# Optimization experiments

Hardware: AMD Instinct MI355X
Metric: run time of the kernel (lower is better)

Reference implementation:

```python
import jax, jax.numpy as jnp
import numpy as np

B, TIN, IN, TRI, D, FFN, L, OUT = 8, 1040, 80, 128, 512, 2048, 8, 1024
H, DH, STRIDE, SEG, RC, LC, MAXMEM = 8, 64, 4, 16, 4, 32, 4
NEG = -1e8
SCALE = DH ** -0.5


def _layer_norm(x, g, b, eps=1e-5):
    m = jnp.mean(x, -1, keepdims=True)
    v = jnp.var(x, -1, keepdims=True)
    return (x - m) * jax.lax.rsqrt(v + eps) * g + b


def _build_attention_mask(U, nseg):
    # Faithful port of Emformer._gen_attention_mask; True = masked out.
    rct = RC * nseg
    mlen = nseg - 1
    rc_rows, q_rows, s_rows = [], [], []
    for i in range(nseg):
        rs, re = i * RC, i * RC + RC
        ss, se = max(i * SEG - LC, 0), min((i + 1) * SEG, U)
        ms = max(i - MAXMEM, 0)
        widths = [ms, i - ms, mlen - i, rs, RC, rct - re, ss, se - ss, U - se]

        def row(allowed):
            return np.concatenate([np.full(max(w, 0), j in allowed, dtype=bool)
                                   for j, w in enumerate(widths)])

        r = row({1, 4, 7})  # memory, own rc block, own (left-extended) segment
        rc_rows.append(np.tile(r, (RC, 1)))
        q_rows.append(np.tile(r, (min(SEG, U - i * SEG), 1)))
        s_rows.append(row({4, 7})[None])  # summary: rc block + segment only
    allow = np.concatenate([np.concatenate(rc_rows), np.concatenate(q_rows), np.concatenate(s_rows)])
    return jnp.asarray(~allow)


def _forward(input, lengths, w_in, ln_in_g, ln_in_b, wq, bq, wk, bk, wv, bv, wo, bo,
             ff_ln_g, ff_ln_b, w1, b1, w2, b2, ln_out_g, ln_out_b, w_out, b_out, lng, lnb):
    x = input @ w_in                                    # (B, TIN, TRI) input_linear (no bias)
    nb, t, _ = x.shape
    nf = t - t % STRIDE
    x = x[:, :nf].reshape(nb, nf // STRIDE, TRI * STRIDE)  # time reduction -> (B, Tr, D)
    lr = lengths // STRIDE
    x = jnp.transpose(x, (1, 0, 2))                     # (Tr, B, D) time-major like torch Emformer
    Tr = x.shape[0]
    U = Tr - RC                                         # utterance length (256)
    nseg = -(-U // SEG)
    utt = x[:U]
    # right-context blocks: hard-copied per segment (last block = trailing rc)
    starts = np.concatenate([np.arange(1, nseg) * SEG, [Tr - RC]])
    idx = (starts[:, None] + np.arange(RC)[None, :]).reshape(-1)
    rc = x[idx]                                         # (nseg*RC, B, D)
    Rt = rc.shape[0]
    Q = Rt + U + nseg                                   # rc + utterance + summary queries
    K = (nseg - 1) + Rt + U                             # mems + rc + utterance keys
    attn_mask = _build_attention_mask(U, nseg)          # (Q, K)
    mems0 = utt.reshape(nseg, SEG, nb, D).mean(1)[:-1]  # AvgPool1d(seg) on raw utterance, drop last
    # padding mask over keys (faithful to _gen_padding_mask)
    rcbl = Q - jnp.max(lr) - nseg
    klen = lr + (nseg - 1) + rcbl
    pad = jnp.arange(K)[None, :] >= klen[:, None]       # (B, K), True = masked

    def step(carry, p):
        utt, rc, mems = carry
        g1, be1, Wq, Bq, Wk, Bk, Wv, Bv, Wo, Bo, g2, be2, Wf1, Bf1, Wf2, Bf2, g3, be3 = p
        ln = _layer_norm(jnp.concatenate([rc, utt]), g1, be1)
        ln_rc, ln_utt = ln[:Rt], ln[Rt:]
        summary = ln_utt.reshape(nseg, SEG, nb, D).mean(1)       # (nseg, B, D)
        qin = jnp.concatenate([ln_rc, ln_utt, summary])          # (Q, B, D)
        kin = jnp.concatenate([mems, ln_rc, ln_utt])             # (K, B, D)
        q = (qin @ Wq + Bq).reshape(Q, nb, H, DH)
        k = (kin @ Wk + Bk).reshape(K, nb, H, DH)
        v = (kin @ Wv + Bv).reshape(K, nb, H, DH)
        w = jnp.einsum('qbhd,kbhd->bhqk', q * SCALE, k)
        w = jnp.where(attn_mask[None, None], NEG, w)
        w = jnp.where(pad[:, None, None, :], NEG, w)
        probs = jax.nn.softmax(w, axis=-1)
        att = jnp.einsum('bhqk,kbhd->qbhd', probs, v).reshape(Q, nb, D)
        out = att @ Wo + Bo
        rcu = out[:Rt + U]
        new_mems = jnp.tanh(out[Rt + U:])[:-1]                   # tanh_on_mem=True, drop last summary
        res = rcu + jnp.concatenate([rc, utt])                   # residual w/ pre-LN input
        h = _layer_norm(res, g2, be2)
        h = jax.nn.relu(h @ Wf1 + Bf1) @ Wf2 + Bf2               # pos_ff (pre-LN inside)
        res = res + h
        res = _layer_norm(res, g3, be3)
        return (res[Rt:], res[:Rt], new_mems), None

    xs = (ln_in_g, ln_in_b, wq, bq, wk, bk, wv, bv, wo, bo,
          ff_ln_g, ff_ln_b, w1, b1, w2, b2, ln_out_g, ln_out_b)
    (utt, rc, mems), _ = jax.lax.scan(step, (utt, rc, mems0), xs)
    y = jnp.transpose(utt, (1, 0, 2))                   # (B, U, D)
    y = _layer_norm(y @ w_out + b_out, lng, lnb)        # output_linear + LayerNorm
    return y, lr


def setup_inputs() -> dict:
    key = jax.random.key(0)
    ks = jax.random.split(key, 12)

    def w(k, shape, fan):
        return jax.random.normal(k, shape, jnp.float32) / np.sqrt(fan)

    return {
        "input": jax.random.normal(ks[0], (B, TIN, IN), jnp.float32),
        "lengths": jax.random.randint(ks[1], (B,), 256, 1025, jnp.int32),
        "w_in": w(ks[2], (IN, TRI), IN),
        "ln_in_g": jnp.ones((L, D), jnp.float32), "ln_in_b": jnp.zeros((L, D), jnp.float32),
        "wq": w(ks[3], (L, D, D), D), "bq": jnp.zeros((L, D), jnp.float32),
        "wk": w(ks[4], (L, D, D), D), "bk": jnp.zeros((L, D), jnp.float32),
        "wv": w(ks[5], (L, D, D), D), "bv": jnp.zeros((L, D), jnp.float32),
        "wo": w(ks[6], (L, D, D), D), "bo": jnp.zeros((L, D), jnp.float32),
        "ff_ln_g": jnp.ones((L, D), jnp.float32), "ff_ln_b": jnp.zeros((L, D), jnp.float32),
        "w1": w(ks[7], (L, D, FFN), D), "b1": jnp.zeros((L, FFN), jnp.float32),
        "w2": w(ks[8], (L, FFN, D), FFN), "b2": jnp.zeros((L, D), jnp.float32),
        "ln_out_g": jnp.ones((L, D), jnp.float32), "ln_out_b": jnp.zeros((L, D), jnp.float32),
        "w_out": w(ks[9], (D, OUT), D), "b_out": jnp.zeros((OUT,), jnp.float32),
        "lng": jnp.ones((OUT,), jnp.float32), "lnb": jnp.zeros((OUT,), jnp.float32),
    }


def reference(input, lengths, w_in, ln_in_g, ln_in_b, wq, bq, wk, bk, wv, bv, wo, bo,
              ff_ln_g, ff_ln_b, w1, b1, w2, b2, ln_out_g, ln_out_b, w_out, b_out, lng, lnb):
    return _forward(input, lengths, w_in, ln_in_g, ln_in_b, wq, bq, wk, bk, wv, bv, wo, bo,
                    ff_ln_g, ff_ln_b, w1, b1, w2, b2, ln_out_g, ln_out_b, w_out, b_out, lng, lnb)
```

## Files before the change

### kernel.cpp

```cpp
#include <hip/hip_runtime.h>
#include <math.h>

#define NB 8
#define D 512
#define H 8
#define DH 64
#define NSEG 16
#define RT 64
#define UU 256
#define QN 336
#define KN 335
#define SROWS 320
#define FFN_D 2048
#define LAYERS 8
#define OUTD 1024
#define TR 260
#define NEGV (-100000000.0f)
#define QSCALE 0.125f

typedef __attribute__((ext_vector_type(8))) short bf16x8;
typedef __attribute__((ext_vector_type(4))) float f32x4;

__device__ inline unsigned short f2bf(float f) {
    union { float f; unsigned int u; } v; v.f = f;
    unsigned int u = v.u;
    unsigned int r = (u + 0x7FFFu + ((u >> 16) & 1u)) >> 16;
    return (unsigned short)r;
}
__device__ inline float bf2f(unsigned short h) {
    union { unsigned int u; float f; } v; v.u = ((unsigned int)h) << 16;
    return v.f;
}

__global__ void lr_k(const int* __restrict__ lengths, int* __restrict__ lrw,
                     float* __restrict__ out_lr) {
    if (threadIdx.x == 0) {
        int mx = 0;
        for (int b = 0; b < NB; ++b) {
            int v = lengths[b] >> 2;
            lrw[b] = v;
            out_lr[b] = (float)v;
            if (v > mx) mx = v;
        }
        lrw[NB] = mx;
    }
}

__global__ __launch_bounds__(128) void inproj_k(const float* __restrict__ input,
                                                const float* __restrict__ w_in,
                                                float* __restrict__ XB) {
    __shared__ float wl[80 * 128];
    __shared__ float il[4 * 80];
    int tid = threadIdx.x;
    int t = blockIdx.x >> 3;
    int b = blockIdx.x & 7;
    for (int i = tid; i < 80 * 128; i += 128) wl[i] = w_in[i];
    const float* inp = input + ((size_t)b * 1040 + (size_t)t * 4) * 80;
    for (int i = tid; i < 320; i += 128) il[i] = inp[i];
    __syncthreads();
    float* xrow = XB + ((size_t)(t * NB + b)) * D;
#pragma unroll
    for (int c = 0; c < 4; ++c) {
        float acc = 0.f;
        for (int i = 0; i < 80; ++i) acc = fmaf(il[c * 80 + i], wl[i * 128 + tid], acc);
        xrow[c * 128 + tid] = acc;
    }
}

__global__ __launch_bounds__(256) void initstate_k(const float* __restrict__ XB,
                                                   float* __restrict__ S) {
    int r = blockIdx.x;
    int srow = r >> 3, b = r & 7;
    int src;
    if (srow < RT) {
        int i = srow >> 2, jj = srow & 3;
        src = (i < 15 ? (i + 1) * 16 : 256) + jj;
    } else {
        src = srow - RT;
    }
    const float* xr = XB + ((size_t)(src * NB + b)) * D;
    float* sr = S + (size_t)r * D;
    sr[threadIdx.x] = xr[threadIdx.x];
    sr[threadIdx.x + 256] = xr[threadIdx.x + 256];
}

__global__ __launch_bounds__(256) void mems0_k(const float* __restrict__ XB,
                                               unsigned short* __restrict__ MEMS) {
    int ib = blockIdx.x;
    int i = ib >> 3, b = ib & 7;
    for (int c = 0; c < 2; ++c) {
        int col = threadIdx.x + c * 256;
        float s = 0.f;
#pragma unroll
        for (int t = 0; t < 16; ++t) s += XB[((size_t)((i * 16 + t) * NB + b)) * D + col];
        MEMS[(size_t)ib * D + col] = f2bf(s * (1.f / 16.f));
    }
}

__global__ __launch_bounds__(256) void ln_k(const float* __restrict__ X,
                                            unsigned short* __restrict__ Y16,
                                            float* __restrict__ Yf,
                                            const float* __restrict__ g,
                                            const float* __restrict__ be, int dual) {
    int row = blockIdx.x;
    const float* x = X + (size_t)row * D;
    float v[2];
    float s = 0.f, ss = 0.f;
#pragma unroll
    for (int j = 0; j < 2; ++j) {
        v[j] = x[threadIdx.x + j * 256];
        s += v[j];
        ss = fmaf(v[j], v[j], ss);
    }
#pragma unroll
    for (int off = 32; off; off >>= 1) {
        s += __shfl_xor(s, off);
        ss += __shfl_xor(ss, off);
    }
    __shared__ float rs_[4], rss_[4];
    int w = threadIdx.x >> 6;
    if ((threadIdx.x & 63) == 0) {
        rs_[w] = s;
        rss_[w] = ss;
    }
    __syncthreads();
    s = rs_[0] + rs_[1] + rs_[2] + rs_[3];
    ss = rss_[0] + rss_[1] + rss_[2] + rss_[3];
    float mean = s * (1.f / D);
    float var = ss * (1.f / D) - mean * mean;
    float rstd = rsqrtf(var + 1e-5f);
#pragma unroll
    for (int j = 0; j < 2; ++j) {
        int col = threadIdx.x + j * 256;
        float y = (v[j] - mean) * rstd * g[col] + be[col];
        Y16[(size_t)row * D + col] = f2bf(y);
        if (dual) Yf[(size_t)row * D + col] = y;
    }
}

__global__ __launch_bounds__(256) void ln_res_k(const float* __restrict__ OUTB,
                                                float* __restrict__ SB,
                                                unsigned short* __restrict__ MEMS,
                                                unsigned short* __restrict__ Y16,
                                                const float* __restrict__ g,
                                                const float* __restrict__ be) {
    int row = blockIdx.x;
    if (row >= SROWS * NB) {
        int j = row - SROWS * NB;
#pragma unroll
        for (int c = 0; c < 2; ++c) {
            int col = threadIdx.x + c * 256;
            MEMS[(size_t)j * D + col] = f2bf(tanhf(OUTB[(size_t)row * D + col]));
        }
        return;
    }
    float v[2];
    float s = 0.f, ss = 0.f;
#pragma unroll
    for (int j = 0; j < 2; ++j) {
        int col = threadIdx.x + j * 256;
        float r = SB[(size_t)row * D + col] + OUTB[(size_t)row * D + col];
        SB[(size_t)row * D + col] = r;
        v[j] = r;
        s += r;
        ss = fmaf(r, r, ss);
    }
#pragma unroll
    for (int off = 32; off; off >>= 1) {
        s += __shfl_xor(s, off);
        ss += __shfl_xor(ss, off);
    }
    __shared__ float rs_[4], rss_[4];
    int w = threadIdx.x >> 6;
    if ((threadIdx.x & 63) == 0) {
        rs_[w] = s;
        rss_[w] = ss;
    }
    __syncthreads();
    s = rs_[0] + rs_[1] + rs_[2] + rs_[3];
    ss = rss_[0] + rss_[1] + rss_[2] + rss_[3];
    float mean = s * (1.f / D);
    float var = ss * (1.f / D) - mean * mean;
    float rstd = rsqrtf(var + 1e-5f);
#pragma unroll
    for (int j = 0; j < 2; ++j) {
        int col = threadIdx.x + j * 256;
        Y16[(size_t)row * D + col] = f2bf((v[j] - mean) * rstd * g[col] + be[col]);
    }
}

__global__ __launch_bounds__(256) void summary_k(const unsigned short* __restrict__ LN16,
                                                 unsigned short* __restrict__ SUM16) {
    int ib = blockIdx.x;
    int i = ib >> 3, b = ib & 7;
    for (int c = 0; c < 2; ++c) {
        int col = threadIdx.x + c * 256;
        float s = 0.f;
#pragma unroll
        for (int t = 0; t < 16; ++t)
            s += bf2f(LN16[((size_t)((RT + i * 16 + t) * NB + b)) * D + col]);
        SUM16[(size_t)ib * D + col] = f2bf(s * (1.f / 16.f));
    }
}

__device__ inline void conv_tile(float (*tile)[33], const float* __restrict__ src, int srcN,
                                 int k0, int sn0, unsigned short* __restrict__ dst, int dstK,
                                 int dn0) {
    int t = threadIdx.x;
    int r = t >> 3, c4 = (t & 7) * 4;
    float4 v = *(const float4*)&src[(size_t)(k0 + r) * srcN + sn0 + c4];
    tile[r][c4 + 0] = v.x;
    tile[r][c4 + 1] = v.y;
    tile[r][c4 + 2] = v.z;
    tile[r][c4 + 3] = v.w;
    __syncthreads();
    ushort4 o;
    o.x = f2bf(tile[c4 + 0][r]);
    o.y = f2bf(tile[c4 + 1][r]);
    o.z = f2bf(tile[c4 + 2][r]);
    o.w = f2bf(tile[c4 + 3][r]);
    *(ushort4*)&dst[(size_t)(dn0 + r) * dstK + k0 + c4] = o;
}

__global__ __launch_bounds__(256) void convw_k(const float* __restrict__ wq,
                                               const float* __restrict__ wk,
                                               const float* __restrict__ wv,
                                               const float* __restrict__ wo,
                                               const float* __restrict__ w1,
                                               const float* __restrict__ w2,
                                               const float* __restrict__ bq,
                                               const float* __restrict__ bk,
                                               const float* __restrict__ bv,
                                               unsigned short* __restrict__ WQKV,
                                               unsigned short* __restrict__ WO16,
                                               unsigned short* __restrict__ W1T,
                                               unsigned short* __restrict__ W2T,
                                               float* __restrict__ BQKV, int l) {
    __shared__ float tile[32][33];
    int t = blockIdx.x;
    if (t == 0) {
        for (int i = threadIdx.x; i < 1536; i += 256)
            BQKV[i] = i < 512 ? bq[l * 512 + i]
                              : (i < 1024 ? bk[l * 512 + i - 512] : bv[l * 512 + i - 1024]);
    }
    if (t < 768) {
        int tn = t % 48, tk = t / 48;
        int n0 = tn * 32, k0 = tk * 32;
        const float* src;
        int sn0;
        if (n0 < 512) { src = wq + (size_t)l * 262144; sn0 = n0; }
        else if (n0 < 1024) { src = wk + (size_t)l * 262144; sn0 = n0 - 512; }
        else { src = wv + (size_t)l * 262144; sn0 = n0 - 1024; }
        conv_tile(tile, src, 512, k0, sn0, WQKV, 512, n0);
    } else if (t < 1024) {
        int tt = t - 768;
        int n0 = (tt % 16) * 32, k0 = (tt / 16) * 32;
        conv_tile(tile, wo + (size_t)l * 262144, 512, k0, n0, WO16, 512, n0);
    } else if (t < 2048) {
        int tt = t - 1024;
        int n0 = (tt % 64) * 32, k0 = (tt / 64) * 32;
        conv_tile(tile, w1 + (size_t)l * 1048576, 2048, k0, n0, W1T, 512, n0);
    } else {
        int tt = t - 2048;
        int n0 = (tt % 16) * 32, k0 = (tt / 16) * 32;
        conv_tile(tile, w2 + (size_t)l * 1048576, 512, k0, n0, W2T, 2048, n0);
    }
}

__global__ __launch_bounds__(256) void convout_k(const float* __restrict__ w_out,
                                                 unsigned short* __restrict__ WOUT16) {
    __shared__ float tile[32][33];
    int t = blockIdx.x;
    int n0 = (t % 32) * 32, k0 = (t / 32) * 32;
    conv_tile(tile, w_out, 1024, k0, n0, WOUT16, 512, n0);
}

__global__ __launch_bounds__(256) void gemm16_k(const unsigned short* __restrict__ A,
                                                const unsigned short* __restrict__ BT,
                                                const float* __restrict__ bias,
                                                void* __restrict__ Cp, int M, int N, int K,
                                                int Kchunk, int flags) {
    __shared__ unsigned short As[2][64][40];
    __shared__ unsigned short Bs[2][64][40];
    int tid = threadIdx.x;
    int wave = tid >> 6, lane = tid & 63;
    int wm = wave >> 1, wn = wave & 1;
    int quad = lane >> 4, sub = lane & 15;
    int m0 = blockIdx.y * 64, n0 = blockIdx.x * 64;
    int kb = blockIdx.z * Kchunk, ke = kb + Kchunk;

    int lrow = tid >> 3, lkc = tid & 7;
    int lrow2 = lrow + 32;
    int lkh = lkc >> 2, lkl = lkc & 3;

    f32x4 acc[2][2] = {};
    int4 ar0, ar1, br0, br1;

    auto loadT = [&](int k0) {
        int gr0 = m0 + lrow, gr1 = m0 + lrow2;
        ar0 = (gr0 < M) ? *(const int4*)&A[(size_t)gr0 * K + k0 + lkc * 8] : make_int4(0, 0, 0, 0);
        ar1 = (gr1 < M) ? *(const int4*)&A[(size_t)gr1 * K + k0 + lkc * 8] : make_int4(0, 0, 0, 0);
        br0 = *(const int4*)&BT[(size_t)(n0 + lrow) * K + k0 + lkc * 8];
        br1 = *(const int4*)&BT[(size_t)(n0 + lrow2) * K + k0 + lkc * 8];
    };
    auto storeT = [&]() {
        *(int4*)&As[lkh][lrow][lkl * 8] = ar0;
        *(int4*)&As[lkh][lrow2][lkl * 8] = ar1;
        *(int4*)&Bs[lkh][lrow][lkl * 8] = br0;
        *(int4*)&Bs[lkh][lrow2][lkl * 8] = br1;
    };
    auto compute = [&]() {
#pragma unroll
        for (int ks = 0; ks < 2; ++ks) {
            bf16x8 af[2], bf[2];
#pragma unroll
            for (int mi = 0; mi < 2; ++mi)
                af[mi] = *(const bf16x8*)&As[ks][wm * 32 + mi * 16 + sub][quad * 8];
#pragma unroll
            for (int ni = 0; ni < 2; ++ni)
                bf[ni] = *(const bf16x8*)&Bs[ks][wn * 32 + ni * 16 + sub][quad * 8];
#pragma unroll
            for (int mi = 0; mi < 2; ++mi)
#pragma unroll
                for (int ni = 0; ni < 2; ++ni)
                    acc[mi][ni] = __builtin_amdgcn_mfma_f32_16x16x32_bf16(af[mi], bf[ni],
                                                                          acc[mi][ni], 0, 0, 0);
        }
    };

    loadT(kb);
    storeT();
    __syncthreads();
    for (int k0 = kb + 64; k0 < ke; k0 += 64) {
        loadT(k0);
        compute();
        __syncthreads();
        storeT();
        __syncthreads();
    }
    compute();

    bool relu = flags & 1, addc = flags & 2, obf = flags & 4, atom = flags & 8;
    bool addbias = !atom || blockIdx.z == 0;
    float* Cf = (float*)Cp;
    unsigned short* Ch = (unsigned short*)Cp;
#pragma unroll
    for (int mi = 0; mi < 2; ++mi) {
#pragma unroll
        for (int ni = 0; ni < 2; ++ni) {
#pragma unroll
            for (int r = 0; r < 4; ++r) {
                int row = m0 + wm * 32 + mi * 16 + quad * 4 + r;
                int col = n0 + wn * 32 + ni * 16 + sub;
                if (row < M) {
                    float v = acc[mi][ni][r] + (addbias ? bias[col] : 0.f);
                    if (relu) v = fmaxf(v, 0.f);
                    size_t idx = (size_t)row * N + col;
                    if (obf) {
                        Ch[idx] = f2bf(v);
                    } else if (atom) {
                        atomicAdd(&Cf[idx], v);
                    } else {
                        if (addc) v += Cf[idx];
                        Cf[idx] = v;
                    }
                }
            }
        }
    }
}

__global__ __launch_bounds__(64) void attn_k(const unsigned short* __restrict__ QKV,
                                             unsigned short* __restrict__ ATT,
                                             const int* __restrict__ lrw) {
    int lane = threadIdx.x;
    int qrow = blockIdx.x;
    int bh = blockIdx.y;
    int b = bh >> 3, h = bh & 7;

    int i, is_sum;
    if (qrow < RT) {
        i = qrow >> 2;
        is_sum = 0;
    } else if (qrow < RT + UU) {
        i = (qrow - RT) >> 4;
        is_sum = 0;
    } else {
        i = qrow - (RT + UU);
        is_sum = 1;
    }
    int ms = (i > 4) ? (i - 4) : 0;
    int n_mem = is_sum ? 0 : (i - ms);
    int us = (i * 16 - 32 > 0) ? (i * 16 - 32) : 0;
    int ue = (i + 1) * 16;
    int total = n_mem + 4 + (ue - us);
    int klen = KN + lrw[b] - lrw[NB];

    __shared__ float qs[64];
    __shared__ float ps[64];
    __shared__ int kks[64];
    qs[lane] = bf2f(QKV[(size_t)(120 + qrow * NB + b) * 1536 + h * DH + lane]) * QSCALE;
    __syncthreads();

    int kk = -1;
    if (lane < total) {
        if (lane < n_mem)
            kk = ms + lane;
        else if (lane < n_mem + 4)
            kk = 15 + i * 4 + (lane - n_mem);
        else
            kk = 79 + us + (lane - n_mem - 4);
    }
    float s = NEGV;
    if (kk >= 0 && kk < klen) {
        const int4* kr = (const int4*)&QKV[(size_t)(kk * NB + b) * 1536 + 512 + h * DH];
        float accd = 0.f;
#pragma unroll
        for (int c = 0; c < 8; ++c) {
            int4 kv = kr[c];
            const int uu[4] = {kv.x, kv.y, kv.z, kv.w};
#pragma unroll
            for (int j = 0; j < 4; ++j) {
                float lo = __uint_as_float(((unsigned)uu[j]) << 16);
                float hi = __uint_as_float(((unsigned)uu[j]) & 0xFFFF0000u);
                accd = fmaf(lo, qs[c * 8 + j * 2], accd);
                accd = fmaf(hi, qs[c * 8 + j * 2 + 1], accd);
            }
        }
        s = accd;
    }
    float m = s;
#pragma unroll
    for (int off = 32; off; off >>= 1) m = fmaxf(m, __shfl_xor(m, off));
    float p = __expf(s - m);
    float sum = p;
#pragma unroll
    for (int off = 32; off; off >>= 1) sum += __shfl_xor(sum, off);
    float inv = 1.f / sum;
    ps[lane] = p * inv;
    kks[lane] = kk;
    __syncthreads();

    float acc = 0.f;
    for (int j = 0; j < total; ++j) {
        int kkj = kks[j];
        acc = fmaf(ps[j], bf2f(QKV[(size_t)(kkj * NB + b) * 1536 + 1024 + h * DH + lane]), acc);
    }
    ATT[(size_t)(qrow * NB + b) * D + h * DH + lane] = f2bf(acc);
}

__global__ __launch_bounds__(256) void final_ln_k(const float* __restrict__ Yb,
                                                  const float* __restrict__ g,
                                                  const float* __restrict__ be,
                                                  float* __restrict__ out) {
    int row = blockIdx.x;
    int u = row >> 3, b = row & 7;
    const float* x = Yb + (size_t)row * OUTD;
    float v[4];
    float s = 0.f, ss = 0.f;
#pragma unroll
    for (int j = 0; j < 4; ++j) {
        v[j] = x[threadIdx.x + j * 256];
        s += v[j];
        ss = fmaf(v[j], v[j], ss);
    }
#pragma unroll
    for (int off = 32; off; off >>= 1) {
        s += __shfl_xor(s, off);
        ss += __shfl_xor(ss, off);
    }
    __shared__ float rs_[4], rss_[4];
    int w = threadIdx.x >> 6;
    if ((threadIdx.x & 63) == 0) {
        rs_[w] = s;
        rss_[w] = ss;
    }
    __syncthreads();
    s = rs_[0] + rs_[1] + rs_[2] + rs_[3];
    ss = rss_[0] + rss_[1] + rss_[2] + rss_[3];
    float mean = s * (1.f / OUTD);
    float var = ss * (1.f / OUTD) - mean * mean;
    float rstd = rsqrtf(var + 1e-5f);
    float* o = out + ((size_t)(b * 256 + u)) * OUTD;
#pragma unroll
    for (int j = 0; j < 4; ++j) {
        int col = threadIdx.x + j * 256;
        o[col] = (v[j] - mean) * rstd * g[col] + be[col];
    }
}

extern "C" void kernel_launch(void* const* d_in, const int* in_sizes, int n_in, void* d_out,
                              int out_size, void* d_ws, size_t ws_size, hipStream_t stream) {
    (void)in_sizes;
    (void)n_in;
    (void)out_size;
    (void)ws_size;
    const float* input = (const float*)d_in[0];
    const int* lengths = (const int*)d_in[1];
    const float* w_in = (const float*)d_in[2];
    const float* ln_in_g = (const float*)d_in[3];
    const float* ln_in_b = (const float*)d_in[4];
    const float* wq = (const float*)d_in[5];
    const float* bq = (const float*)d_in[6];
    const float* wk = (const float*)d_in[7];
    const float* bk = (const float*)d_in[8];
    const float* wv = (const float*)d_in[9];
    const float* bv = (const float*)d_in[10];
    const float* wo = (const float*)d_in[11];
    const float* bo = (const float*)d_in[12];
    const float* ff_g = (const float*)d_in[13];
    const float* ff_b = (const float*)d_in[14];
    const float* w1 = (const float*)d_in[15];
    const float* b1 = (const float*)d_in[16];
    const float* w2 = (const float*)d_in[17];
    const float* b2 = (const float*)d_in[18];
    const float* lo_g = (const float*)d_in[19];
    const float* lo_b = (const float*)d_in[20];
    const float* w_out = (const float*)d_in[21];
    const float* b_out = (const float*)d_in[22];
    const float* lng = (const float*)d_in[23];
    const float* lnb = (const float*)d_in[24];
    float* out = (float*)d_out;

    char* wsc = (char*)d_ws;
    size_t off = 0;
    auto alloc = [&](size_t bytes) {
        char* p = wsc + off;
        off += (bytes + 255) & ~(size_t)255;
        return p;
    };
    unsigned short* ACT16 = (unsigned short*)alloc(2808ULL * 512 * 2);
    unsigned short* ATT16 = (unsigned short*)alloc(2688ULL * 512 * 2);
    unsigned short* HB16 = (unsigned short*)alloc(2560ULL * 2048 * 2);
    unsigned short* QKVB = (unsigned short*)alloc(2808ULL * 1536 * 2);
    float* SB = (float*)alloc(2560ULL * 512 * 4);
    unsigned short* WQKV16 = (unsigned short*)alloc(1536ULL * 512 * 2);
    unsigned short* WO16 = (unsigned short*)alloc(512ULL * 512 * 2);
    unsigned short* W1T = (unsigned short*)alloc(2048ULL * 512 * 2);
    unsigned short* W2T = (unsigned short*)alloc(512ULL * 2048 * 2);
    unsigned short* WOUT16 = (unsigned short*)alloc(1024ULL * 512 * 2);
    float* BQKV = (float*)alloc(1536 * 4);
    int* LRW = (int*)alloc(64);

    unsigned short* MEMS16 = ACT16;
    unsigned short* LNB16 = ACT16 + 120 * 512;
    unsigned short* SUMB16 = ACT16 + 2680 * 512;
    float* XB = (float*)QKVB;
    float* OUTB = (float*)QKVB;
    float* HBf = (float*)QKVB;

    lr_k<<<1, 64, 0, stream>>>(lengths, LRW, out + (size_t)NB * 256 * 1024);
    convout_k<<<512, 256, 0, stream>>>(w_out, WOUT16);
    inproj_k<<<TR * NB, 128, 0, stream>>>(input, w_in, XB);
    initstate_k<<<SROWS * NB, 256, 0, stream>>>(XB, SB);
    mems0_k<<<15 * NB, 256, 0, stream>>>(XB, MEMS16);

    for (int l = 0; l < LAYERS; ++l) {
        convw_k<<<3072, 256, 0, stream>>>(wq, wk, wv, wo, w1, w2, bq, bk, bv, WQKV16, WO16, W1T,
                                          W2T, BQKV, l);
        ln_k<<<SROWS * NB, 256, 0, stream>>>(SB, LNB16, SB, ln_in_g + l * D, ln_in_b + l * D, 0);
        summary_k<<<NSEG * NB, 256, 0, stream>>>(LNB16, SUMB16);
        gemm16_k<<<dim3(24, 44, 1), 256, 0, stream>>>(ACT16, WQKV16, BQKV, QKVB, 2808, 1536, 512,
                                                      512, 4);
        attn_k<<<dim3(QN, NB * H), 64, 0, stream>>>(QKVB, ATT16, LRW);
        gemm16_k<<<dim3(8, 42, 1), 256, 0, stream>>>(ATT16, WO16, bo + l * D, OUTB, QN * NB, D,
                                                     D, D, 0);
        ln_res_k<<<(SROWS + 15) * NB, 256, 0, stream>>>(OUTB, SB, MEMS16, LNB16, ff_g + l * D,
                                                        ff_b + l * D);
        gemm16_k<<<dim3(32, 40, 1), 256, 0, stream>>>(LNB16, W1T, b1 + l * FFN_D, HB16,
                                                      SROWS * NB, FFN_D, D, D, 1 | 4);
        gemm16_k<<<dim3(8, 40, 4), 256, 0, stream>>>(HB16, W2T, b2 + l * D, SB, SROWS * NB, D,
                                                     FFN_D, 512, 8);
        ln_k<<<SROWS * NB, 256, 0, stream>>>(SB, LNB16, SB, lo_g + l * D, lo_b + l * D, 1);
    }
    gemm16_k<<<dim3(16, 32, 1), 256, 0, stream>>>(LNB16 + (size_t)RT * NB * D, WOUT16, b_out,
                                                  HBf, UU * NB, OUTD, D, D, 0);
    final_ln_k<<<UU * NB, 256, 0, stream>>>(HBf, lng, lnb, out);
}
```

Before: 1.276 ms.

## Merge all heads into one 256-thread attention block per query row and batch

After: 1.196 ms. 6.3% less time.

```diff
diff --git a/kernel.cpp b/kernel.cpp
--- a/kernel.cpp
+++ b/kernel.cpp
@@ -370,13 +370,12 @@
     }
 }
 
-__global__ __launch_bounds__(64) void attn_k(const unsigned short* __restrict__ QKV,
-                                             unsigned short* __restrict__ ATT,
-                                             const int* __restrict__ lrw) {
-    int lane = threadIdx.x;
+__global__ __launch_bounds__(256) void attn_k(const unsigned short* __restrict__ QKV,
+                                              unsigned short* __restrict__ ATT,
+                                              const int* __restrict__ lrw) {
+    int tid = threadIdx.x;
     int qrow = blockIdx.x;
-    int bh = blockIdx.y;
-    int b = bh >> 3, h = bh & 7;
+    int b = blockIdx.y;
 
     int i, is_sum;
     if (qrow < RT) {
@@ -396,57 +395,93 @@
     int total = n_mem + 4 + (ue - us);
     int klen = KN + lrw[b] - lrw[NB];
 
-    __shared__ float qs[64];
-    __shared__ float ps[64];
+    __shared__ float qs[512];
+    __shared__ float sc[H][64];
     __shared__ int kks[64];
-    qs[lane] = bf2f(QKV[(size_t)(120 + qrow * NB + b) * 1536 + h * DH + lane]) * QSCALE;
-    __syncthreads();
-
-    int kk = -1;
-    if (lane < total) {
-        if (lane < n_mem)
-            kk = ms + lane;
-        else if (lane < n_mem + 4)
-            kk = 15 + i * 4 + (lane - n_mem);
-        else
-            kk = 79 + us + (lane - n_mem - 4);
-    }
-    float s = NEGV;
-    if (kk >= 0 && kk < klen) {
-        const int4* kr = (const int4*)&QKV[(size_t)(kk * NB + b) * 1536 + 512 + h * DH];
-        float accd = 0.f;
-#pragma unroll
-        for (int c = 0; c < 8; ++c) {
-            int4 kv = kr[c];
-            const int uu[4] = {kv.x, kv.y, kv.z, kv.w};
-#pragma unroll
-            for (int j = 0; j < 4; ++j) {
-                float lo = __uint_as_float(((unsigned)uu[j]) << 16);
-                float hi = __uint_as_float(((unsigned)uu[j]) & 0xFFFF0000u);
-                accd = fmaf(lo, qs[c * 8 + j * 2], accd);
-                accd = fmaf(hi, qs[c * 8 + j * 2 + 1], accd);
+
+    {
+        const unsigned int* qrp =
+            (const unsigned int*)&QKV[(size_t)(120 + qrow * NB + b) * 1536];
+        unsigned int u = qrp[tid];
+        qs[2 * tid] = __uint_as_float(u << 16) * QSCALE;
+        qs[2 * tid + 1] = __uint_as_float(u & 0xFFFF0000u) * QSCALE;
+    }
+    if (tid < 64) {
+        int kk = -1;
+        if (tid < total) {
+            if (tid < n_mem)
+                kk = ms + tid;
+            else if (tid < n_mem + 4)
+                kk = 15 + i * 4 + (tid - n_mem);
+            else
+                kk = 79 + us + (tid - n_mem - 4);
+        }
+        kks[tid] = kk;
+    }
+    __syncthreads();
+
+#pragma unroll
+    for (int rep = 0; rep < 2; ++rep) {
+        int p = rep * 256 + tid;
+        int h = p >> 6, j = p & 63;
+        int kk = kks[j];
+        float s = NEGV;
+        if (kk >= 0 && kk < klen) {
+            const int4* kr = (const int4*)&QKV[(size_t)(kk * NB + b) * 1536 + 512 + h * DH];
+            const float* qh = &qs[h * DH];
+            float accd = 0.f;
+#pragma unroll
+            for (int c = 0; c < 8; ++c) {
+                int4 kv = kr[c];
+                const int uu[4] = {kv.x, kv.y, kv.z, kv.w};
+#pragma unroll
+                for (int jj = 0; jj < 4; ++jj) {
+                    float lo = __uint_as_float(((unsigned)uu[jj]) << 16);
+                    float hi = __uint_as_float(((unsigned)uu[jj]) & 0xFFFF0000u);
+                    accd = fmaf(lo, qh[c * 8 + jj * 2], accd);
+                    accd = fmaf(hi, qh[c * 8 + jj * 2 + 1], accd);
+                }
             }
-        }
-        s = accd;
-    }
-    float m = s;
-#pragma unroll
-    for (int off = 32; off; off >>= 1) m = fmaxf(m, __shfl_xor(m, off));
-    float p = __expf(s - m);
-    float sum = p;
-#pragma unroll
-    for (int off = 32; off; off >>= 1) sum += __shfl_xor(sum, off);
-    float inv = 1.f / sum;
-    ps[lane] = p * inv;
-    kks[lane] = kk;
-    __syncthreads();
-
-    float acc = 0.f;
-    for (int j = 0; j < total; ++j) {
-        int kkj = kks[j];
-        acc = fmaf(ps[j], bf2f(QKV[(size_t)(kkj * NB + b) * 1536 + 1024 + h * DH + lane]), acc);
-    }
-    ATT[(size_t)(qrow * NB + b) * D + h * DH + lane] = f2bf(acc);
+            s = accd;
+        }
+        sc[h][j] = s;
+    }
+    __syncthreads();
+
+    {
+        int wv = tid >> 6, lane = tid & 63;
+#pragma unroll
+        for (int hh = 0; hh < 2; ++hh) {
+            int h = wv + hh * 4;
+            float s = sc[h][lane];
+            float m = s;
+#pragma unroll
+            for (int off = 32; off; off >>= 1) m = fmaxf(m, __shfl_xor(m, off));
+            float p = __expf(s - m);
+            float sum = p;
+#pragma unroll
+            for (int off = 32; off; off >>= 1) sum += __shfl_xor(sum, off);
+            sc[h][lane] = p / sum;
+        }
+    }
+    __syncthreads();
+
+    {
+        int h = tid >> 5;
+        const float* ph = sc[h];
+        float a0 = 0.f, a1 = 0.f;
+        const unsigned short* vbase = QKV + (size_t)b * 1536 + 1024 + 2 * tid;
+#pragma unroll 4
+        for (int j = 0; j < total; ++j) {
+            int kkj = kks[j];
+            unsigned int u = *(const unsigned int*)&vbase[(size_t)kkj * (NB * 1536)];
+            float p = ph[j];
+            a0 = fmaf(p, __uint_as_float(u << 16), a0);
+            a1 = fmaf(p, __uint_as_float(u & 0xFFFF0000u), a1);
+        }
+        unsigned int o = ((unsigned int)f2bf(a0)) | (((unsigned int)f2bf(a1)) << 16);
+        *(unsigned int*)&ATT[(size_t)(qrow * NB + b) * D + 2 * tid] = o;
+    }
 }
 
 __global__ __launch_bounds__(256) void final_ln_k(const float* __restrict__ Yb,
@@ -562,7 +597,7 @@
         summary_k<<<NSEG * NB, 256, 0, stream>>>(LNB16, SUMB16);
         gemm16_k<<<dim3(24, 44, 1), 256, 0, stream>>>(ACT16, WQKV16, BQKV, QKVB, 2808, 1536, 512,
                                                       512, 4);
-        attn_k<<<dim3(QN, NB * H), 64, 0, stream>>>(QKVB, ATT16, LRW);
+        attn_k<<<dim3(QN, NB), 256, 0, stream>>>(QKVB, ATT16, LRW);
         gemm16_k<<<dim3(8, 42, 1), 256, 0, stream>>>(ATT16, WO16, bo + l * D, OUTB, QN * NB, D,
                                                      D, D, 0);
         ln_res_k<<<(SROWS + 15) * NB, 256, 0, stream>>>(OUTB, SB, MEMS16, LNB16, ff_g + l * D,
```
